# Kernel tuning notes

Hardware: AMD Instinct MI355X
Metric: run time of the kernel (lower is better)

Reference implementation:

```python
import jax, jax.numpy as jnp
import numpy as np

B, C, H, W = 4, 256, 64, 64
EMB = C // 8  # embedding_channels = inChannels // k


def _conv1x1(x, w, b):
    # x: [B, Cin, H, W], w: [Cout, Cin], b: [Cout] -> [B, Cout, H, W]
    return jnp.einsum('oi,bihw->bohw', w, x) + b[None, :, None, None]


def setup_inputs() -> dict:
    key = jax.random.key(0)
    ks = jax.random.split(key, 10)
    s = 0.05
    return {
        'x': jax.random.normal(ks[0], (B, C, H, W), dtype=jnp.float32),
        'key_w': jax.random.normal(ks[1], (EMB, C), dtype=jnp.float32) * s,
        'key_b': jax.random.normal(ks[2], (EMB,), dtype=jnp.float32) * s,
        'query_w': jax.random.normal(ks[3], (EMB, C), dtype=jnp.float32) * s,
        'query_b': jax.random.normal(ks[4], (EMB,), dtype=jnp.float32) * s,
        'value_w': jax.random.normal(ks[5], (EMB, C), dtype=jnp.float32) * s,
        'value_b': jax.random.normal(ks[6], (EMB,), dtype=jnp.float32) * s,
        'att_w': jax.random.normal(ks[7], (C, EMB), dtype=jnp.float32) * s,
        'att_b': jax.random.normal(ks[8], (C,), dtype=jnp.float32) * s,
        'gamma': jnp.zeros((), dtype=jnp.float32),
    }


def reference(x, key_w, key_b, query_w, query_b, value_w, value_b, att_w, att_b, gamma):
    b, c, h, w = x.shape
    n = h * w
    f = _conv1x1(x, key_w, key_b).reshape(b, -1, n)    # [B, E, N]
    g = _conv1x1(x, query_w, query_b).reshape(b, -1, n)  # [B, E, N]
    hh = _conv1x1(x, value_w, value_b).reshape(b, -1, n)  # [B, E, N]
    # s[b,i,j] = sum_e f[b,e,i] * g[b,e,j]
    s = jnp.einsum('bei,bej->bij', f, g)  # [B, N, N]
    # NOTE: softmax over dim=1 (the i / key-index axis), NOT the last dim
    beta = jax.nn.softmax(s, axis=1)
    v = jnp.einsum('bei,bij->bej', hh, beta).reshape(b, -1, h, w)  # [B, E, H, W]
    o = _conv1x1(v, att_w, att_b)  # [B, C, H, W]
    y = gamma * o + x
    return (y, o)
```

## Files before the change

kernel.cpp:

```cpp
#include <hip/hip_runtime.h>
#include <hip/hip_bf16.h>
#include <math.h>

#define BB 4
#define CC 256
#define NN 4096
#define EE 32

typedef __attribute__((ext_vector_type(8))) short bf16x8;
typedef __attribute__((ext_vector_type(4))) float f32x4;
typedef __attribute__((ext_vector_type(16))) float f32x16;
typedef __attribute__((ext_vector_type(2))) unsigned uint32x2_t;

__device__ inline unsigned short f2bf(float x) {
    union { __hip_bfloat16 h; unsigned short u; } cv;
    cv.h = __float2bfloat16(x);
    return cv.u;
}
__device__ inline unsigned pk2(float lo, float hi) {
    return ((unsigned)f2bf(hi) << 16) | (unsigned)f2bf(lo);
}
__device__ inline float fexp2(float x) { return __builtin_amdgcn_exp2f(x); }
__device__ inline unsigned cvtpk(float lo, float hi) {
    unsigned r;
    asm("v_cvt_pk_bf16_f32 %0, %1, %2" : "=v"(r) : "v"(lo), "v"(hi));
    return r;
}

__global__ __launch_bounds__(256) void wcvt_kernel(
    const float* __restrict__ kw, const float* __restrict__ kb,
    const float* __restrict__ qw, const float* __restrict__ qb,
    const float* __restrict__ vw, const float* __restrict__ vb,
    __hip_bfloat16* __restrict__ wB, float* __restrict__ bB)
{
    int r = blockIdx.x;
    int t = threadIdx.x;
    int rr = r & 31;
    const float* src; float scale = 1.f;
    if (r < 32)      src = kw;
    else if (r < 64) { src = qw; scale = 1.44269504f; }
    else             src = vw;
    if (t < 64) {
        float4 v = *(const float4*)(src + rr * 256 + t * 4);
        uint2 p;
        p.x = pk2(v.x * scale, v.y * scale);
        p.y = pk2(v.z * scale, v.w * scale);
        *(uint2*)((unsigned short*)wB + r * 256 + t * 4) = p;
    }
    if (r == 0 && t >= 64 && t < 160) {
        int e = t - 64;
        const float* bs = (e < 32) ? kb : ((e < 64) ? qb : vb);
        float sc = (e >= 32 && e < 64) ? 1.44269504f : 1.f;
        bB[e] = bs[e & 31] * sc;
    }
}

__global__ __launch_bounds__(256) void proj_kernel(
    const float* __restrict__ x,
    const __hip_bfloat16* __restrict__ wB, const float* __restrict__ bB,
    __hip_bfloat16* __restrict__ fT, __hip_bfloat16* __restrict__ gT,
    __hip_bfloat16* __restrict__ hT)
{
    __shared__ unsigned xs[32][132];
    int b     = blockIdx.x >> 7;
    int ibase = (blockIdx.x & 127) << 5;
    int wv    = threadIdx.x >> 6;
    int l     = threadIdx.x & 63;
    int il    = l & 31;
    int pg    = (wv << 1) | (l >> 5);

    const float* xb = x + (size_t)b * CC * NN + ibase + il;
#pragma unroll
    for (int j = 0; j < 16; ++j) {
        int p = pg + (j << 3);
        float lo = xb[(size_t)(2 * p) * NN];
        float hi = xb[(size_t)(2 * p + 1) * NN];
        xs[il][p] = pk2(lo, hi);
    }
    __syncthreads();

    int q15  = l & 15, g = l >> 4;
    int isub = wv & 1, eh = wv >> 1;
    int irow = (isub << 4) + q15;
    const __hip_bfloat16* w0 = wB + ((size_t)(eh * 48) + q15) * 256;

    f32x4 a0 = {0,0,0,0}, a1 = {0,0,0,0}, a2 = {0,0,0,0};
#pragma unroll
    for (int kk = 0; kk < 8; ++kk) {
        bf16x8 Bf = *(const bf16x8*)&xs[irow][kk * 16 + 4 * g];
        int co = kk * 32 + 8 * g;
        bf16x8 A0 = *(const bf16x8*)(w0 + co);
        bf16x8 A1 = *(const bf16x8*)(w0 + 16 * 256 + co);
        bf16x8 A2 = *(const bf16x8*)(w0 + 32 * 256 + co);
        a0 = __builtin_amdgcn_mfma_f32_16x16x32_bf16(A0, Bf, a0, 0, 0, 0);
        a1 = __builtin_amdgcn_mfma_f32_16x16x32_bf16(A1, Bf, a1, 0, 0, 0);
        a2 = __builtin_amdgcn_mfma_f32_16x16x32_bf16(A2, Bf, a2, 0, 0, 0);
    }

    int ig = ibase + irow;
    auto emit = [&](f32x4 acc, int T) {
        float4 bb = *(const float4*)(bB + T * 16 + 4 * g);
        float d0 = acc[0] + bb.x, d1 = acc[1] + bb.y;
        float d2 = acc[2] + bb.z, d3 = acc[3] + bb.w;
        if (T < 4) {
            __hip_bfloat16* dst = (T < 2) ? fT : gT;
            int eoff = ((T & 1) << 4) + 4 * g;
            uint2 pq; pq.x = pk2(d0, d1); pq.y = pk2(d2, d3);
            *(uint2*)((unsigned short*)dst + ((size_t)b * NN + ig) * EE + eoff) = pq;
        } else {
            unsigned short* dst = (unsigned short*)hT;
            int e = ((T - 4) << 4) + 4 * g;
            size_t base = ((size_t)b * EE + e) * NN + ig;
            dst[base]          = f2bf(d0);
            dst[base + NN]     = f2bf(d1);
            dst[base + 2 * NN] = f2bf(d2);
            dst[base + 3 * NN] = f2bf(d3);
        }
    };
    emit(a0, eh * 3 + 0);
    emit(a1, eh * 3 + 1);
    emit(a2, eh * 3 + 2);
}

__global__ __launch_bounds__(512, 4) void attn_kernel(
    const __hip_bfloat16* __restrict__ fT,
    const __hip_bfloat16* __restrict__ gT,
    const __hip_bfloat16* __restrict__ hT,
    float* __restrict__ vT)
{
    int b     = blockIdx.x >> 7;
    int qbase = (blockIdx.x & 127) * 32;
    int wv    = threadIdx.x >> 6;
    int lane  = threadIdx.x & 63;
    int q     = lane & 31;
    int h     = lane >> 5;

    const __hip_bfloat16* fb = fT + (size_t)b * NN * EE;
    const __hip_bfloat16* gb = gT + (size_t)b * NN * EE;
    const __hip_bfloat16* hb = hT + (size_t)b * EE * NN + (size_t)q * NN;

    bf16x8 Qf0 = *(const bf16x8*)(gb + (size_t)(qbase + q) * EE + 8 * h);
    bf16x8 Qf1 = *(const bf16x8*)(gb + (size_t)(qbase + q) * EE + 16 + 8 * h);

    float l = 0.f;
    f32x16 O = {0,0,0,0,0,0,0,0,0,0,0,0,0,0,0,0};
    const f32x16 z16 = {0,0,0,0,0,0,0,0,0,0,0,0,0,0,0,0};

    int k0 = wv * 512;
    bf16x8 K0 = *(const bf16x8*)(fb + (size_t)(k0 + q) * EE + 8 * h);
    bf16x8 K1 = *(const bf16x8*)(fb + (size_t)(k0 + q) * EE + 16 + 8 * h);
    bf16x8 V0 = *(const bf16x8*)(hb + k0 + 8 * h);
    bf16x8 V1 = *(const bf16x8*)(hb + k0 + 16 + 8 * h);

    for (int c = 0; c < 16; ++c) {
        int kn = (k0 + 32) & (NN - 1);
        bf16x8 nK0 = *(const bf16x8*)(fb + (size_t)(kn + q) * EE + 8 * h);
        bf16x8 nK1 = *(const bf16x8*)(fb + (size_t)(kn + q) * EE + 16 + 8 * h);
        bf16x8 nV0 = *(const bf16x8*)(hb + kn + 8 * h);
        bf16x8 nV1 = *(const bf16x8*)(hb + kn + 16 + 8 * h);

        __builtin_amdgcn_s_setprio(1);
        f32x16 S = __builtin_amdgcn_mfma_f32_32x32x16_bf16(K0, Qf0, z16, 0, 0, 0);
        S = __builtin_amdgcn_mfma_f32_32x32x16_bf16(K1, Qf1, S, 0, 0, 0);
        __builtin_amdgcn_s_setprio(0);

        float p[16];
#pragma unroll
        for (int r = 0; r < 16; ++r) p[r] = fexp2(S[r]);
        float s0 = (p[0] + p[1]) + (p[2] + p[3]);
        float s1 = (p[4] + p[5]) + (p[6] + p[7]);
        float s2 = (p[8] + p[9]) + (p[10] + p[11]);
        float s3 = (p[12] + p[13]) + (p[14] + p[15]);
        l += (s0 + s1) + (s2 + s3);

        unsigned j0 = cvtpk(p[0], p[1]),   j1 = cvtpk(p[2], p[3]);
        unsigned j2 = cvtpk(p[4], p[5]),   j3 = cvtpk(p[6], p[7]);
        unsigned j4 = cvtpk(p[8], p[9]),   j5 = cvtpk(p[10], p[11]);
        unsigned j6 = cvtpk(p[12], p[13]), j7 = cvtpk(p[14], p[15]);

        uint32x2_t sA = __builtin_amdgcn_permlane32_swap(j0, j2, false, false);
        uint32x2_t sB = __builtin_amdgcn_permlane32_swap(j1, j3, false, false);
        union { unsigned u[4]; bf16x8 v; } P1;
        P1.u[0] = sA.x; P1.u[1] = sB.x; P1.u[2] = sA.y; P1.u[3] = sB.y;
        uint32x2_t sC = __builtin_amdgcn_permlane32_swap(j4, j6, false, false);
        uint32x2_t sD = __builtin_amdgcn_permlane32_swap(j5, j7, false, false);
        union { unsigned u[4]; bf16x8 v; } P2;
        P2.u[0] = sC.x; P2.u[1] = sD.x; P2.u[2] = sC.y; P2.u[3] = sD.y;

        __builtin_amdgcn_s_setprio(1);
        O = __builtin_amdgcn_mfma_f32_32x32x16_bf16(V0, P1.v, O, 0, 0, 0);
        O = __builtin_amdgcn_mfma_f32_32x32x16_bf16(V1, P2.v, O, 0, 0, 0);
        __builtin_amdgcn_s_setprio(0);

        K0 = nK0; K1 = nK1; V0 = nV0; V1 = nV1;
        k0 += 32;
    }

    __shared__ float slx[8][64];
    __shared__ float sO[8][64][17];
    slx[wv][lane] = l;
#pragma unroll
    for (int r = 0; r < 16; ++r) sO[wv][lane][r] = O[r];
    __syncthreads();

    if (wv == 0) {
        float L = 0.f;
        float Of[16];
#pragma unroll
        for (int r = 0; r < 16; ++r) Of[r] = 0.f;
#pragma unroll
        for (int w = 0; w < 8; ++w) {
            L += slx[w][lane];
#pragma unroll
            for (int r = 0; r < 16; ++r) Of[r] += sO[w][lane][r];
        }
        L += __shfl_xor(L, 32, 64);
        float inv = 1.f / L;
        float* vp = vT + ((size_t)b * NN + qbase + q) * EE;
#pragma unroll
        for (int gi = 0; gi < 4; ++gi) {
            f32x4 ov;
#pragma unroll
            for (int r = 0; r < 4; ++r) ov[r] = Of[4 * gi + r] * inv;
            *(f32x4*)(vp + 8 * gi + 4 * h) = ov;
        }
    }
}

__global__ __launch_bounds__(256) void out_kernel(
    const float* __restrict__ vT, const float* __restrict__ aw,
    const float* __restrict__ ab, const float* __restrict__ x,
    const float* __restrict__ gamma_p,
    float* __restrict__ y, float* __restrict__ o)
{
    int blk    = blockIdx.x;
    int csplit = blk & 15;
    int itile  = (blk >> 4) & 15;
    int b      = blk >> 8;
    int i      = itile * 256 + threadIdx.x;
    float gm   = gamma_p[0];

    const float4* vp4 = (const float4*)(vT + ((size_t)b * NN + i) * EE);
    float vr[EE];
#pragma unroll
    for (int u = 0; u < 8; ++u) {
        float4 t = vp4[u];
        vr[4*u+0] = t.x; vr[4*u+1] = t.y; vr[4*u+2] = t.z; vr[4*u+3] = t.w;
    }

    int co0 = csplit * 16;
#pragma unroll
    for (int co = co0; co < co0 + 16; ++co) {
        float s = ab[co];
#pragma unroll
        for (int e = 0; e < EE; ++e)
            s = fmaf(aw[co * EE + e], vr[e], s);
        size_t idx = ((size_t)b * CC + co) * NN + i;
        o[idx] = s;
        y[idx] = fmaf(gm, s, x[idx]);
    }
}

extern "C" void kernel_launch(void* const* d_in, const int* in_sizes, int n_in,
                              void* d_out, int out_size, void* d_ws, size_t ws_size,
                              hipStream_t stream)
{
    const float* x  = (const float*)d_in[0];
    const float* kw = (const float*)d_in[1];
    const float* kb = (const float*)d_in[2];
    const float* qw = (const float*)d_in[3];
    const float* qb = (const float*)d_in[4];
    const float* vw = (const float*)d_in[5];
    const float* vb = (const float*)d_in[6];
    const float* aw = (const float*)d_in[7];
    const float* ab = (const float*)d_in[8];
    const float* gm = (const float*)d_in[9];

    float* y = (float*)d_out;
    float* o = y + (size_t)BB * CC * NN;

    float*          vT = (float*)d_ws;
    float*          bB = vT + (size_t)BB * NN * EE;
    __hip_bfloat16* wB = (__hip_bfloat16*)(bB + 128);
    __hip_bfloat16* fT = wB + 96 * 256;
    __hip_bfloat16* gT = fT + (size_t)BB * NN * EE;
    __hip_bfloat16* hT = gT + (size_t)BB * NN * EE;

    wcvt_kernel<<<96, 256, 0, stream>>>(kw, kb, qw, qb, vw, vb, wB, bB);
    proj_kernel<<<BB * (NN / 32), 256, 0, stream>>>(x, wB, bB, fT, gT, hT);
    attn_kernel<<<BB * (NN / 32), 512, 0, stream>>>(fT, gT, hT, vT);
    out_kernel<<<BB * 16 * 16, 256, 0, stream>>>(vT, aw, ab, x, gm, y, o);
}
```

Before: 60.68 us.

## Fuse output projection into attention kernel with 1024-thread blocks

The separate out_kernel is folded into the attention kernel. Each 1024-thread block handles 64 queries, using two query groups of eight key-split waves. Partial O accumulators are packed to bf16 in shared memory before reduction, and the normalized v rows are staged in LDS so all threads compute the 256-channel output projection and the residual. This removes the vT workspace round-trip and one launch, but reduces the attention grid to 256 blocks, adds bf16 rounding to the partial sums, and makes the output phase run inside the attention blocks.

```diff
diff --git a/kernel.cpp b/kernel.cpp
--- a/kernel.cpp
+++ b/kernel.cpp
@@ -25,6 +25,12 @@
     unsigned r;
     asm("v_cvt_pk_bf16_f32 %0, %1, %2" : "=v"(r) : "v"(lo), "v"(hi));
     return r;
+}
+__device__ inline float bflo(unsigned u) {
+    union { unsigned v; float f; } c; c.v = u << 16; return c.f;
+}
+__device__ inline float bfhi(unsigned u) {
+    union { unsigned v; float f; } c; c.v = u & 0xFFFF0000u; return c.f;
 }
 
 __global__ __launch_bounds__(256) void wcvt_kernel(
@@ -122,18 +128,23 @@
     emit(a2, eh * 3 + 2);
 }
 
-__global__ __launch_bounds__(512, 4) void attn_kernel(
+__global__ __launch_bounds__(1024, 4) void attn_kernel(
     const __hip_bfloat16* __restrict__ fT,
     const __hip_bfloat16* __restrict__ gT,
     const __hip_bfloat16* __restrict__ hT,
-    float* __restrict__ vT)
-{
-    int b     = blockIdx.x >> 7;
-    int qbase = (blockIdx.x & 127) * 32;
+    const float* __restrict__ aw, const float* __restrict__ ab,
+    const float* __restrict__ x,  const float* __restrict__ gamma_p,
+    float* __restrict__ y, float* __restrict__ o)
+{
+    int b     = blockIdx.x >> 6;
+    int ibase = (blockIdx.x & 63) << 6;
     int wv    = threadIdx.x >> 6;
     int lane  = threadIdx.x & 63;
+    int qg    = wv >> 3;
+    int ks    = wv & 7;
     int q     = lane & 31;
     int h     = lane >> 5;
+    int qbase = ibase + qg * 32;
 
     const __hip_bfloat16* fb = fT + (size_t)b * NN * EE;
     const __hip_bfloat16* gb = gT + (size_t)b * NN * EE;
@@ -146,7 +157,7 @@
     f32x16 O = {0,0,0,0,0,0,0,0,0,0,0,0,0,0,0,0};
     const f32x16 z16 = {0,0,0,0,0,0,0,0,0,0,0,0,0,0,0,0};
 
-    int k0 = wv * 512;
+    int k0 = ks * 512;
     bf16x8 K0 = *(const bf16x8*)(fb + (size_t)(k0 + q) * EE + 8 * h);
     bf16x8 K1 = *(const bf16x8*)(fb + (size_t)(k0 + q) * EE + 16 + 8 * h);
     bf16x8 V0 = *(const bf16x8*)(hb + k0 + 8 * h);
@@ -193,68 +204,57 @@
         __builtin_amdgcn_s_setprio(0);
 
         K0 = nK0; K1 = nK1; V0 = nV0; V1 = nV1;
-        k0 += 32;
-    }
-
-    __shared__ float slx[8][64];
-    __shared__ float sO[8][64][17];
+        k0 = kn;
+    }
+
+    __shared__ unsigned sOp[16][64][9];
+    __shared__ float    slx[16][64];
+    __shared__ float    vbuf[64][33];
     slx[wv][lane] = l;
 #pragma unroll
-    for (int r = 0; r < 16; ++r) sO[wv][lane][r] = O[r];
+    for (int r = 0; r < 8; ++r) sOp[wv][lane][r] = cvtpk(O[2*r], O[2*r+1]);
     __syncthreads();
 
-    if (wv == 0) {
+    if (ks == 0) {
         float L = 0.f;
         float Of[16];
 #pragma unroll
         for (int r = 0; r < 16; ++r) Of[r] = 0.f;
 #pragma unroll
         for (int w = 0; w < 8; ++w) {
-            L += slx[w][lane];
-#pragma unroll
-            for (int r = 0; r < 16; ++r) Of[r] += sO[w][lane][r];
+            L += slx[wv + w][lane];
+#pragma unroll
+            for (int r = 0; r < 8; ++r) {
+                unsigned u = sOp[wv + w][lane][r];
+                Of[2*r]   += bflo(u);
+                Of[2*r+1] += bfhi(u);
+            }
         }
         L += __shfl_xor(L, 32, 64);
         float inv = 1.f / L;
-        float* vp = vT + ((size_t)b * NN + qbase + q) * EE;
-#pragma unroll
-        for (int gi = 0; gi < 4; ++gi) {
-            f32x4 ov;
-#pragma unroll
-            for (int r = 0; r < 4; ++r) ov[r] = Of[4 * gi + r] * inv;
-            *(f32x4*)(vp + 8 * gi + 4 * h) = ov;
-        }
-    }
-}
-
-__global__ __launch_bounds__(256) void out_kernel(
-    const float* __restrict__ vT, const float* __restrict__ aw,
-    const float* __restrict__ ab, const float* __restrict__ x,
-    const float* __restrict__ gamma_p,
-    float* __restrict__ y, float* __restrict__ o)
-{
-    int blk    = blockIdx.x;
-    int csplit = blk & 15;
-    int itile  = (blk >> 4) & 15;
-    int b      = blk >> 8;
-    int i      = itile * 256 + threadIdx.x;
-    float gm   = gamma_p[0];
-
-    const float4* vp4 = (const float4*)(vT + ((size_t)b * NN + i) * EE);
-    float vr[EE];
-#pragma unroll
-    for (int u = 0; u < 8; ++u) {
-        float4 t = vp4[u];
-        vr[4*u+0] = t.x; vr[4*u+1] = t.y; vr[4*u+2] = t.z; vr[4*u+3] = t.w;
-    }
-
-    int co0 = csplit * 16;
-#pragma unroll
-    for (int co = co0; co < co0 + 16; ++co) {
+        int pos = qg * 32 + q;
+#pragma unroll
+        for (int gi = 0; gi < 4; ++gi)
+#pragma unroll
+            for (int r = 0; r < 4; ++r)
+                vbuf[pos][8 * gi + 4 * h + r] = Of[4 * gi + r] * inv;
+    }
+    __syncthreads();
+
+    int pos = threadIdx.x & 63;
+    int cog = threadIdx.x >> 6;
+    float gm = gamma_p[0];
+    float vv[EE];
+#pragma unroll
+    for (int e = 0; e < EE; ++e) vv[e] = vbuf[pos][e];
+    int i = ibase + pos;
+#pragma unroll
+    for (int j = 0; j < 16; ++j) {
+        int co = cog * 16 + j;
         float s = ab[co];
 #pragma unroll
         for (int e = 0; e < EE; ++e)
-            s = fmaf(aw[co * EE + e], vr[e], s);
+            s = fmaf(aw[co * EE + e], vv[e], s);
         size_t idx = ((size_t)b * CC + co) * NN + i;
         o[idx] = s;
         y[idx] = fmaf(gm, s, x[idx]);
@@ -279,8 +279,7 @@
     float* y = (float*)d_out;
     float* o = y + (size_t)BB * CC * NN;
 
-    float*          vT = (float*)d_ws;
-    float*          bB = vT + (size_t)BB * NN * EE;
+    float*          bB = (float*)d_ws;
     __hip_bfloat16* wB = (__hip_bfloat16*)(bB + 128);
     __hip_bfloat16* fT = wB + 96 * 256;
     __hip_bfloat16* gT = fT + (size_t)BB * NN * EE;
@@ -288,6 +287,6 @@
 
     wcvt_kernel<<<96, 256, 0, stream>>>(kw, kb, qw, qb, vw, vb, wB, bB);
     proj_kernel<<<BB * (NN / 32), 256, 0, stream>>>(x, wB, bB, fT, gT, hT);
-    attn_kernel<<<BB * (NN / 32), 512, 0, stream>>>(fT, gT, hT, vT);
-    out_kernel<<<BB * 16 * 16, 256, 0, stream>>>(vT, aw, ab, x, gm, y, o);
-}
+    attn_kernel<<<BB * (NN / 64), 1024, 0, stream>>>(
+        fT, gT, hT, aw, ab, x, gm, y, o);
+}
```

Result: slower. 65.28 us (+7.6%).

## Process two query tiles per wave and tile value layout for contiguous loads

Applied to the files above, without the earlier changes.

The attention kernel now handles 64 query columns per block with 16 waves, each wave covering 256 keys and reusing the loaded K and V fragments for two 32-column query tiles. The value tensor is stored in a per-32-key tiled layout so each V fragment load is contiguous. Partial outputs are packed to bf16 before the cross-wave shared-memory reduction to cut LDS size. The aim is to halve global K/V traffic per query, at the cost of more registers per wave, 1024-thread blocks, and some extra rounding in the partial sums.

```diff
diff --git a/kernel.cpp b/kernel.cpp
--- a/kernel.cpp
+++ b/kernel.cpp
@@ -25,6 +25,12 @@
     unsigned r;
     asm("v_cvt_pk_bf16_f32 %0, %1, %2" : "=v"(r) : "v"(lo), "v"(hi));
     return r;
+}
+__device__ inline float bflo(unsigned u) {
+    union { unsigned v; float f; } c; c.v = u << 16; return c.f;
+}
+__device__ inline float bfhi(unsigned u) {
+    union { unsigned v; float f; } c; c.v = u & 0xFFFF0000u; return c.f;
 }
 
 __global__ __launch_bounds__(256) void wcvt_kernel(
@@ -109,12 +115,13 @@
             *(uint2*)((unsigned short*)dst + ((size_t)b * NN + ig) * EE + eoff) = pq;
         } else {
             unsigned short* dst = (unsigned short*)hT;
-            int e = ((T - 4) << 4) + 4 * g;
-            size_t base = ((size_t)b * EE + e) * NN + ig;
-            dst[base]          = f2bf(d0);
-            dst[base + NN]     = f2bf(d1);
-            dst[base + 2 * NN] = f2bf(d2);
-            dst[base + 3 * NN] = f2bf(d3);
+            int e  = ((T - 4) << 4) + 4 * g;
+            int kt = ig >> 5, kk2 = ig & 31;
+            size_t base = ((size_t)(b * 128 + kt) * 32 + e) * 32 + kk2;
+            dst[base]       = f2bf(d0);
+            dst[base + 32]  = f2bf(d1);
+            dst[base + 64]  = f2bf(d2);
+            dst[base + 96]  = f2bf(d3);
         }
     };
     emit(a0, eh * 3 + 0);
@@ -122,14 +129,14 @@
     emit(a2, eh * 3 + 2);
 }
 
-__global__ __launch_bounds__(512, 4) void attn_kernel(
+__global__ __launch_bounds__(1024, 4) void attn_kernel(
     const __hip_bfloat16* __restrict__ fT,
     const __hip_bfloat16* __restrict__ gT,
     const __hip_bfloat16* __restrict__ hT,
     float* __restrict__ vT)
 {
-    int b     = blockIdx.x >> 7;
-    int qbase = (blockIdx.x & 127) * 32;
+    int b     = blockIdx.x >> 6;
+    int ibase = (blockIdx.x & 63) << 6;
     int wv    = threadIdx.x >> 6;
     int lane  = threadIdx.x & 63;
     int q     = lane & 31;
@@ -137,86 +144,121 @@
 
     const __hip_bfloat16* fb = fT + (size_t)b * NN * EE;
     const __hip_bfloat16* gb = gT + (size_t)b * NN * EE;
-    const __hip_bfloat16* hb = hT + (size_t)b * EE * NN + (size_t)q * NN;
-
-    bf16x8 Qf0 = *(const bf16x8*)(gb + (size_t)(qbase + q) * EE + 8 * h);
-    bf16x8 Qf1 = *(const bf16x8*)(gb + (size_t)(qbase + q) * EE + 16 + 8 * h);
-
-    float l = 0.f;
-    f32x16 O = {0,0,0,0,0,0,0,0,0,0,0,0,0,0,0,0};
+    const __hip_bfloat16* hb = hT + (size_t)b * NN * EE + q * 32 + 8 * h;
+
+    bf16x8 Qa0 = *(const bf16x8*)(gb + (size_t)(ibase + q) * EE + 8 * h);
+    bf16x8 Qa1 = *(const bf16x8*)(gb + (size_t)(ibase + q) * EE + 16 + 8 * h);
+    bf16x8 Qb0 = *(const bf16x8*)(gb + (size_t)(ibase + 32 + q) * EE + 8 * h);
+    bf16x8 Qb1 = *(const bf16x8*)(gb + (size_t)(ibase + 32 + q) * EE + 16 + 8 * h);
+
+    float lA = 0.f, lB = 0.f;
+    f32x16 OA = {0,0,0,0,0,0,0,0,0,0,0,0,0,0,0,0};
+    f32x16 OB = {0,0,0,0,0,0,0,0,0,0,0,0,0,0,0,0};
     const f32x16 z16 = {0,0,0,0,0,0,0,0,0,0,0,0,0,0,0,0};
 
-    int k0 = wv * 512;
+    int k0 = wv * 256;
     bf16x8 K0 = *(const bf16x8*)(fb + (size_t)(k0 + q) * EE + 8 * h);
     bf16x8 K1 = *(const bf16x8*)(fb + (size_t)(k0 + q) * EE + 16 + 8 * h);
-    bf16x8 V0 = *(const bf16x8*)(hb + k0 + 8 * h);
-    bf16x8 V1 = *(const bf16x8*)(hb + k0 + 16 + 8 * h);
-
-    for (int c = 0; c < 16; ++c) {
+
+    for (int c = 0; c < 8; ++c) {
         int kn = (k0 + 32) & (NN - 1);
         bf16x8 nK0 = *(const bf16x8*)(fb + (size_t)(kn + q) * EE + 8 * h);
         bf16x8 nK1 = *(const bf16x8*)(fb + (size_t)(kn + q) * EE + 16 + 8 * h);
-        bf16x8 nV0 = *(const bf16x8*)(hb + kn + 8 * h);
-        bf16x8 nV1 = *(const bf16x8*)(hb + kn + 16 + 8 * h);
+        bf16x8 V0  = *(const bf16x8*)(hb + (size_t)k0 * 32);
+        bf16x8 V1  = *(const bf16x8*)(hb + (size_t)k0 * 32 + 16);
 
         __builtin_amdgcn_s_setprio(1);
-        f32x16 S = __builtin_amdgcn_mfma_f32_32x32x16_bf16(K0, Qf0, z16, 0, 0, 0);
-        S = __builtin_amdgcn_mfma_f32_32x32x16_bf16(K1, Qf1, S, 0, 0, 0);
+        f32x16 SA = __builtin_amdgcn_mfma_f32_32x32x16_bf16(K0, Qa0, z16, 0, 0, 0);
+        SA = __builtin_amdgcn_mfma_f32_32x32x16_bf16(K1, Qa1, SA, 0, 0, 0);
         __builtin_amdgcn_s_setprio(0);
 
-        float p[16];
-#pragma unroll
-        for (int r = 0; r < 16; ++r) p[r] = fexp2(S[r]);
-        float s0 = (p[0] + p[1]) + (p[2] + p[3]);
-        float s1 = (p[4] + p[5]) + (p[6] + p[7]);
-        float s2 = (p[8] + p[9]) + (p[10] + p[11]);
-        float s3 = (p[12] + p[13]) + (p[14] + p[15]);
-        l += (s0 + s1) + (s2 + s3);
-
-        unsigned j0 = cvtpk(p[0], p[1]),   j1 = cvtpk(p[2], p[3]);
-        unsigned j2 = cvtpk(p[4], p[5]),   j3 = cvtpk(p[6], p[7]);
-        unsigned j4 = cvtpk(p[8], p[9]),   j5 = cvtpk(p[10], p[11]);
-        unsigned j6 = cvtpk(p[12], p[13]), j7 = cvtpk(p[14], p[15]);
-
-        uint32x2_t sA = __builtin_amdgcn_permlane32_swap(j0, j2, false, false);
-        uint32x2_t sB = __builtin_amdgcn_permlane32_swap(j1, j3, false, false);
-        union { unsigned u[4]; bf16x8 v; } P1;
-        P1.u[0] = sA.x; P1.u[1] = sB.x; P1.u[2] = sA.y; P1.u[3] = sB.y;
-        uint32x2_t sC = __builtin_amdgcn_permlane32_swap(j4, j6, false, false);
-        uint32x2_t sD = __builtin_amdgcn_permlane32_swap(j5, j7, false, false);
-        union { unsigned u[4]; bf16x8 v; } P2;
-        P2.u[0] = sC.x; P2.u[1] = sD.x; P2.u[2] = sC.y; P2.u[3] = sD.y;
+        {
+            float p[16];
+#pragma unroll
+            for (int r = 0; r < 16; ++r) p[r] = fexp2(SA[r]);
+            lA += ((p[0]+p[1])+(p[2]+p[3])) + ((p[4]+p[5])+(p[6]+p[7]))
+                + ((p[8]+p[9])+(p[10]+p[11])) + ((p[12]+p[13])+(p[14]+p[15]));
+            unsigned j0 = cvtpk(p[0], p[1]),   j1 = cvtpk(p[2], p[3]);
+            unsigned j2 = cvtpk(p[4], p[5]),   j3 = cvtpk(p[6], p[7]);
+            unsigned j4 = cvtpk(p[8], p[9]),   j5 = cvtpk(p[10], p[11]);
+            unsigned j6 = cvtpk(p[12], p[13]), j7 = cvtpk(p[14], p[15]);
+            uint32x2_t sA2 = __builtin_amdgcn_permlane32_swap(j0, j2, false, false);
+            uint32x2_t sB2 = __builtin_amdgcn_permlane32_swap(j1, j3, false, false);
+            union { unsigned u[4]; bf16x8 v; } P1;
+            P1.u[0] = sA2.x; P1.u[1] = sB2.x; P1.u[2] = sA2.y; P1.u[3] = sB2.y;
+            uint32x2_t sC2 = __builtin_amdgcn_permlane32_swap(j4, j6, false, false);
+            uint32x2_t sD2 = __builtin_amdgcn_permlane32_swap(j5, j7, false, false);
+            union { unsigned u[4]; bf16x8 v; } P2;
+            P2.u[0] = sC2.x; P2.u[1] = sD2.x; P2.u[2] = sC2.y; P2.u[3] = sD2.y;
+            __builtin_amdgcn_s_setprio(1);
+            OA = __builtin_amdgcn_mfma_f32_32x32x16_bf16(V0, P1.v, OA, 0, 0, 0);
+            OA = __builtin_amdgcn_mfma_f32_32x32x16_bf16(V1, P2.v, OA, 0, 0, 0);
+            __builtin_amdgcn_s_setprio(0);
+        }
 
         __builtin_amdgcn_s_setprio(1);
-        O = __builtin_amdgcn_mfma_f32_32x32x16_bf16(V0, P1.v, O, 0, 0, 0);
-        O = __builtin_amdgcn_mfma_f32_32x32x16_bf16(V1, P2.v, O, 0, 0, 0);
+        f32x16 SB = __builtin_amdgcn_mfma_f32_32x32x16_bf16(K0, Qb0, z16, 0, 0, 0);
+        SB = __builtin_amdgcn_mfma_f32_32x32x16_bf16(K1, Qb1, SB, 0, 0, 0);
         __builtin_amdgcn_s_setprio(0);
 
-        K0 = nK0; K1 = nK1; V0 = nV0; V1 = nV1;
-        k0 += 32;
-    }
-
-    __shared__ float slx[8][64];
-    __shared__ float sO[8][64][17];
-    slx[wv][lane] = l;
-#pragma unroll
-    for (int r = 0; r < 16; ++r) sO[wv][lane][r] = O[r];
+        {
+            float p[16];
+#pragma unroll
+            for (int r = 0; r < 16; ++r) p[r] = fexp2(SB[r]);
+            lB += ((p[0]+p[1])+(p[2]+p[3])) + ((p[4]+p[5])+(p[6]+p[7]))
+                + ((p[8]+p[9])+(p[10]+p[11])) + ((p[12]+p[13])+(p[14]+p[15]));
+            unsigned j0 = cvtpk(p[0], p[1]),   j1 = cvtpk(p[2], p[3]);
+            unsigned j2 = cvtpk(p[4], p[5]),   j3 = cvtpk(p[6], p[7]);
+            unsigned j4 = cvtpk(p[8], p[9]),   j5 = cvtpk(p[10], p[11]);
+            unsigned j6 = cvtpk(p[12], p[13]), j7 = cvtpk(p[14], p[15]);
+            uint32x2_t sA2 = __builtin_amdgcn_permlane32_swap(j0, j2, false, false);
+            uint32x2_t sB2 = __builtin_amdgcn_permlane32_swap(j1, j3, false, false);
+            union { unsigned u[4]; bf16x8 v; } P1;
+            P1.u[0] = sA2.x; P1.u[1] = sB2.x; P1.u[2] = sA2.y; P1.u[3] = sB2.y;
+            uint32x2_t sC2 = __builtin_amdgcn_permlane32_swap(j4, j6, false, false);
+            uint32x2_t sD2 = __builtin_amdgcn_permlane32_swap(j5, j7, false, false);
+            union { unsigned u[4]; bf16x8 v; } P2;
+            P2.u[0] = sC2.x; P2.u[1] = sD2.x; P2.u[2] = sC2.y; P2.u[3] = sD2.y;
+            __builtin_amdgcn_s_setprio(1);
+            OB = __builtin_amdgcn_mfma_f32_32x32x16_bf16(V0, P1.v, OB, 0, 0, 0);
+            OB = __builtin_amdgcn_mfma_f32_32x32x16_bf16(V1, P2.v, OB, 0, 0, 0);
+            __builtin_amdgcn_s_setprio(0);
+        }
+
+        K0 = nK0; K1 = nK1;
+        k0 = kn;
+    }
+
+    __shared__ unsigned sOp[16][64][17];
+    __shared__ float    slx[16][64][2];
+    slx[wv][lane][0] = lA;
+    slx[wv][lane][1] = lB;
+#pragma unroll
+    for (int r = 0; r < 8; ++r) {
+        sOp[wv][lane][r]     = cvtpk(OA[2*r], OA[2*r+1]);
+        sOp[wv][lane][8 + r] = cvtpk(OB[2*r], OB[2*r+1]);
+    }
     __syncthreads();
 
-    if (wv == 0) {
+    if (wv < 2) {
+        int set = wv;
         float L = 0.f;
         float Of[16];
 #pragma unroll
         for (int r = 0; r < 16; ++r) Of[r] = 0.f;
 #pragma unroll
-        for (int w = 0; w < 8; ++w) {
-            L += slx[w][lane];
-#pragma unroll
-            for (int r = 0; r < 16; ++r) Of[r] += sO[w][lane][r];
+        for (int w = 0; w < 16; ++w) {
+            L += slx[w][lane][set];
+#pragma unroll
+            for (int r = 0; r < 8; ++r) {
+                unsigned u = sOp[w][lane][set * 8 + r];
+                Of[2*r]   += bflo(u);
+                Of[2*r+1] += bfhi(u);
+            }
         }
         L += __shfl_xor(L, 32, 64);
         float inv = 1.f / L;
-        float* vp = vT + ((size_t)b * NN + qbase + q) * EE;
+        float* vp = vT + ((size_t)b * NN + ibase + set * 32 + q) * EE;
 #pragma unroll
         for (int gi = 0; gi < 4; ++gi) {
             f32x4 ov;
@@ -288,6 +330,6 @@
 
     wcvt_kernel<<<96, 256, 0, stream>>>(kw, kb, qw, qb, vw, vb, wB, bB);
     proj_kernel<<<BB * (NN / 32), 256, 0, stream>>>(x, wB, bB, fT, gT, hT);
-    attn_kernel<<<BB * (NN / 32), 512, 0, stream>>>(fT, gT, hT, vT);
+    attn_kernel<<<BB * (NN / 64), 1024, 0, stream>>>(fT, gT, hT, vT);
     out_kernel<<<BB * 16 * 16, 256, 0, stream>>>(vT, aw, ab, x, gm, y, o);
 }
```

After: 62.13 us. 1.02x slower.
